# Optimization experiments

Measured on AMD Instinct MI355X. Metric: run time of the kernel, lower is better.

Reference implementation:

```python
import jax, jax.numpy as jnp
from jax import lax
import numpy as np

B, C, H, W = 32, 3, 224, 224
NUM_CLASSES = 100
K = 3  # kernel size
OUT1 = 32


def _bn(x, g, b, m, v, eps=1e-5):
    # eval-mode batchnorm over channel dim of NCHW
    inv = g / jnp.sqrt(v + eps)
    return x * inv[None, :, None, None] + (b - m * inv)[None, :, None, None]


def _conv(x, w, pad=1):
    return lax.conv_general_dilated(
        x, w, (1, 1), ((pad, pad), (pad, pad)),
        dimension_numbers=('NCHW', 'OIHW', 'NCHW'))


def _maxpool2(x):
    return lax.reduce_window(x, -jnp.inf, lax.max, (1, 1, 2, 2), (1, 1, 2, 2), 'VALID')


def setup_inputs() -> dict:
    key = jax.random.key(0)
    ks = jax.random.split(key, 32)
    n = lambda k, s, sc=0.05: jax.random.normal(k, s, jnp.float32) * sc
    u = lambda k, s: jax.random.uniform(k, s, jnp.float32, 0.5, 1.5)
    inp = {
        'x': jax.random.normal(ks[0], (B, C, H, W), jnp.float32),
        # weight_gen MLP: Linear(3,128)->ReLU->Linear(128,256)->ReLU->Linear(256, 32*3*3*3)
        'w1': n(ks[1], (128, C)), 'b1': n(ks[2], (128,)),
        'w2': n(ks[3], (256, 128)), 'b2': n(ks[4], (256,)),
        'w3': n(ks[5], (OUT1 * C * K * K, 256)), 'b3': n(ks[6], (OUT1 * C * K * K,)),
        # bias_gen: Linear(3, 32)
        'wb': n(ks[7], (OUT1, C)), 'bb': n(ks[8], (OUT1,)),
        'conv2_w': n(ks[9], (64, 32, 3, 3)), 'conv2_b': n(ks[10], (64,)),
        'conv3_w': n(ks[11], (128, 64, 3, 3)), 'conv3_b': n(ks[12], (128,)),
        'bn1_g': 1.0 + n(ks[13], (32,)), 'bn1_b': n(ks[14], (32,)), 'bn1_m': n(ks[15], (32,)), 'bn1_v': u(ks[16], (32,)),
        'bn2_g': 1.0 + n(ks[17], (64,)), 'bn2_b': n(ks[18], (64,)), 'bn2_m': n(ks[19], (64,)), 'bn2_v': u(ks[20], (64,)),
        'bn3_g': 1.0 + n(ks[21], (128,)), 'bn3_b': n(ks[22], (128,)), 'bn3_m': n(ks[23], (128,)), 'bn3_v': u(ks[24], (128,)),
        'fc_w': n(ks[25], (NUM_CLASSES, 128)), 'fc_b': n(ks[26], (NUM_CLASSES,)),
    }
    return inp


def reference(x, w1, b1, w2, b2, w3, b3, wb, bb, conv2_w, conv2_b, conv3_w, conv3_b,
              bn1_g, bn1_b, bn1_m, bn1_v, bn2_g, bn2_b, bn2_m, bn2_v,
              bn3_g, bn3_b, bn3_m, bn3_v, fc_w, fc_b):
    Bx = x.shape[0]
    # DynamicConv2D: channel indicator is all-ones since C == max_in_channels
    ind = jnp.ones((Bx, C), x.dtype)
    h = jax.nn.relu(ind @ w1.T + b1)
    h = jax.nn.relu(h @ w2.T + b2)
    dyn_w = (h @ w3.T + b3).reshape(Bx, OUT1, C, K, K)  # per-sample [O,I,k,k]
    dyn_b = ind @ wb.T + bb                             # per-sample [O]
    # vmap over batch: one single-image conv per sample with its own weights
    y = jax.vmap(lambda xi, wi, bi: _conv(xi[None], wi)[0] + bi[:, None, None])(x, dyn_w, dyn_b)
    y = jax.nn.relu(_bn(y, bn1_g, bn1_b, bn1_m, bn1_v))
    y = _maxpool2(y)
    y = jax.nn.relu(_bn(_conv(y, conv2_w) + conv2_b[None, :, None, None], bn2_g, bn2_b, bn2_m, bn2_v))
    y = _maxpool2(y)
    y = jax.nn.relu(_bn(_conv(y, conv3_w) + conv3_b[None, :, None, None], bn3_g, bn3_b, bn3_m, bn3_v))
    y = y.mean(axis=(2, 3))  # AdaptiveAvgPool2d((1,1)) + flatten
    # dropout is identity in eval
    return y @ fc_w.T + fc_b
```

## Files before the change

kernel.cpp:

```cpp
#include <hip/hip_runtime.h>
#include <hip/hip_bf16.h>

#define BATCH 32
#define HW1 224

typedef __attribute__((ext_vector_type(8))) short short8;
typedef __attribute__((ext_vector_type(4))) float floatx4;

static __device__ __forceinline__ unsigned short f2bf(float f) {
    unsigned int u = __float_as_uint(f);
    unsigned int r = (u + 0x7fffu + ((u >> 16) & 1u)) >> 16;
    return (unsigned short)r;
}

typedef __attribute__((address_space(1))) const unsigned int guint;
typedef __attribute__((address_space(3))) unsigned int suint;
static __device__ __forceinline__ void gload_lds16(const void* g, void* l) {
    __builtin_amdgcn_global_load_lds((guint*)g, (suint*)l, 16, 0, 0);
}

__global__ __launch_bounds__(256) void gen_dynw_repack(
    const float* __restrict__ w1, const float* __restrict__ b1,
    const float* __restrict__ w2, const float* __restrict__ b2,
    const float* __restrict__ w3, const float* __restrict__ b3,
    const float* __restrict__ conv2_w, const float* __restrict__ conv3_w,
    const float* __restrict__ wb, const float* __restrict__ bb,
    const float* __restrict__ conv2_b, const float* __restrict__ conv3_b,
    const float* __restrict__ bn1_g, const float* __restrict__ bn1_b,
    const float* __restrict__ bn1_m, const float* __restrict__ bn1_v,
    const float* __restrict__ bn2_g, const float* __restrict__ bn2_b,
    const float* __restrict__ bn2_m, const float* __restrict__ bn2_v,
    const float* __restrict__ bn3_g, const float* __restrict__ bn3_b,
    const float* __restrict__ bn3_m, const float* __restrict__ bn3_v,
    float* __restrict__ dwt,
    unsigned short* __restrict__ wrep2, unsigned short* __restrict__ wrep3,
    float* __restrict__ bn1_s, float* __restrict__ bn1_t,
    float* __restrict__ bn2_s, float* __restrict__ bn2_t,
    float* __restrict__ bn3_s, float* __restrict__ bn3_t,
    float* __restrict__ feat)
{
    __shared__ float h1s[128];
    __shared__ float h2s[256];
    const int blk = blockIdx.x;
    const int t = threadIdx.x;
    if (blk < 216) {
        if (t < 128) {
            float s = b1[t] + w1[t*3+0] + w1[t*3+1] + w1[t*3+2];
            h1s[t] = fmaxf(s, 0.f);
        }
        __syncthreads();
        {
            float s0 = b2[t], s1 = 0.f, s2 = 0.f, s3 = 0.f;
            const float* wr = w2 + (size_t)t*128;
#pragma unroll 4
            for (int k = 0; k < 128; k += 4) {
                float4 wv = *(const float4*)(wr + k);
                s0 = fmaf(wv.x, h1s[k  ], s0);
                s1 = fmaf(wv.y, h1s[k+1], s1);
                s2 = fmaf(wv.z, h1s[k+2], s2);
                s3 = fmaf(wv.w, h1s[k+3], s3);
            }
            h2s[t] = fmaxf((s0 + s1) + (s2 + s3), 0.f);
        }
        __syncthreads();
        const int wave = t >> 6, lane = t & 63;
        const int row = blk*4 + wave;
        float4 wv = *(const float4*)(w3 + (size_t)row*256 + lane*4);
        float4 hv = *(const float4*)&h2s[lane*4];
        float s = wv.x*hv.x + wv.y*hv.y + wv.z*hv.z + wv.w*hv.w;
#pragma unroll
        for (int m = 1; m < 64; m <<= 1) s += __shfl_xor(s, m);
        if (lane == 0) {
            int oc = row / 27, tap = row - oc*27;
            dwt[tap*32 + oc] = s + b3[row];
        }
    } else if (blk < 576) {
        const int i = (blk - 216)*256 + t;
        const int N2 = 9*64*32;
        if (i < N2) {
            int tp = i / (64*32); int rem = i - tp*(64*32);
            int oc = rem >> 5, ic = rem & 31;
            wrep2[i] = f2bf(conv2_w[(oc*32 + ic)*9 + tp]);
        } else {
            int j = i - N2;
            int tp = j / (128*64); int rem = j - tp*(128*64);
            int oc = rem >> 6, ic = rem & 63;
            wrep3[j] = f2bf(conv3_w[(oc*64 + ic)*9 + tp]);
        }
    } else {
        if (t < 32) {
            float dynb = bb[t] + wb[t*3+0] + wb[t*3+1] + wb[t*3+2];
            float s = bn1_g[t] / sqrtf(bn1_v[t] + 1e-5f);
            bn1_s[t] = s;
            bn1_t[t] = (dynb - bn1_m[t]) * s + bn1_b[t];
        }
        if (t < 64) {
            float s = bn2_g[t] / sqrtf(bn2_v[t] + 1e-5f);
            bn2_s[t] = s;
            bn2_t[t] = (conv2_b[t] - bn2_m[t]) * s + bn2_b[t];
        }
        if (t < 128) {
            float s = bn3_g[t] / sqrtf(bn3_v[t] + 1e-5f);
            bn3_s[t] = s;
            bn3_t[t] = (conv3_b[t] - bn3_m[t]) * s + bn3_b[t];
        }
        for (int i = t; i < BATCH*128; i += 256) feat[i] = 0.f;
    }
}

__global__ __launch_bounds__(256) void conv1_pool(
    const float* __restrict__ x, const float* __restrict__ dwt,
    const float* __restrict__ bn_s, const float* __restrict__ bn_t,
    unsigned short* __restrict__ act1)
{
    __shared__ __align__(16) unsigned short sp[18*18*4];
    __shared__ __align__(16) unsigned short swA[32*32];
    __shared__ __align__(16) unsigned short swB[32*32];

    const int tid = threadIdx.x;
    const int bx = blockIdx.x, by = blockIdx.y, b = blockIdx.z;
    const int gx0 = bx*16 - 1, gy0 = by*16 - 1;
    const float* xb = x + (size_t)b * 3 * HW1 * HW1;

    for (int i = tid; i < 1024; i += 256) { swA[i] = 0; swB[i] = 0; }

    float v[2][3];
#pragma unroll
    for (int k = 0; k < 2; ++k) {
        int i = tid + k*256;
        v[k][0] = 0.f; v[k][1] = 0.f; v[k][2] = 0.f;
        if (i < 324) {
            int r = i / 18, c = i - r*18;
            int gy = gy0 + r, gx = gx0 + c;
            if ((unsigned)gy < HW1 && (unsigned)gx < HW1) {
                const float* pp = xb + gy*HW1 + gx;
                v[k][0] = pp[0];
                v[k][1] = pp[HW1*HW1];
                v[k][2] = pp[2*HW1*HW1];
            }
        }
    }
#pragma unroll
    for (int k = 0; k < 2; ++k) {
        int i = tid + k*256;
        if (i < 324) {
            unsigned int lo = (unsigned int)f2bf(v[k][0]) |
                              ((unsigned int)f2bf(v[k][1]) << 16);
            unsigned int hi = (unsigned int)f2bf(v[k][2]);
            *(uint2*)&sp[i*4] = make_uint2(lo, hi);
        }
    }
    __syncthreads();

#pragma unroll
    for (int k = 0; k < 4; ++k) {
        int i = tid + k*256;
        if (i < 864) {
            int tap = i >> 5, oc = i & 31;
            int ic = tap / 9, kk = tap - ic*9;
            int ky = kk / 3, kx = kk - ky*3;
            unsigned short w = f2bf(dwt[i]);
            if (kk == 8)      swB[oc*32 + ic] = w;
            else if (kx < 2)  swA[oc*32 + ky*8 + kx*4 + ic] = w;
            else              swA[oc*32 + 3*8  + ky*4 + ic] = w;
        }
    }
    __syncthreads();

    const int lane = tid & 63, wave = tid >> 6;
    const int n = lane & 15, quad = lane >> 4;

    short8 afrA[2], afrB[2];
#pragma unroll
    for (int h = 0; h < 2; ++h) {
        afrA[h] = *(const short8*)&swA[((h*16 + n)*32) + quad*8];
        afrB[h] = *(const short8*)&swB[((h*16 + n)*32) + quad*8];
    }
    float4 sv[2], tv[2];
#pragma unroll
    for (int h = 0; h < 2; ++h) {
        sv[h] = *(const float4*)(bn_s + h*16 + quad*4);
        tv[h] = *(const float4*)(bn_t + h*16 + quad*4);
    }

    union U { short8 s8; uint2 u2[2]; };

    const int y0w = wave*4;
    float ev[2][4];

#pragma unroll
    for (int yi = 0; yi < 4; ++yi) {
        const int y = y0w + yi;
        int r0 = (quad < 3) ? (y + quad) : y;
        int c0 = (quad < 3) ? n : (n + 2);
        int r1 = (quad < 3) ? (y + quad) : (y + 1);
        int c1 = (quad < 3) ? (n + 1) : (n + 2);
        U bf1;
        bf1.u2[0] = *(const uint2*)&sp[(r0*18 + c0)*4];
        bf1.u2[1] = *(const uint2*)&sp[(r1*18 + c1)*4];
        U bf2;
        bf2.u2[0] = *(const uint2*)&sp[((y+2)*18 + (n+2))*4];
        bf2.u2[1] = bf2.u2[0];

        float vr[2][4];
#pragma unroll
        for (int h = 0; h < 2; ++h) {
            floatx4 acc = {0.f, 0.f, 0.f, 0.f};
            acc = __builtin_amdgcn_mfma_f32_16x16x32_bf16(afrA[h], bf1.s8, acc, 0, 0, 0);
            acc = __builtin_amdgcn_mfma_f32_16x16x32_bf16(afrB[h], bf2.s8, acc, 0, 0, 0);
            float sj[4] = {sv[h].x, sv[h].y, sv[h].z, sv[h].w};
            float tj[4] = {tv[h].x, tv[h].y, tv[h].z, tv[h].w};
#pragma unroll
            for (int j = 0; j < 4; ++j)
                vr[h][j] = fmaxf(fmaf(acc[j], sj[j], tj[j]), 0.f);
        }

        if ((yi & 1) == 0) {
#pragma unroll
            for (int h = 0; h < 2; ++h)
#pragma unroll
                for (int j = 0; j < 4; ++j) ev[h][j] = vr[h][j];
        } else {
            int py = by*8 + ((y0w + yi) >> 1);
            int px = bx*8 + (n >> 1);
            unsigned short* dstp =
                act1 + ((size_t)((b*112 + py)*112 + px))*32 + quad*4;
#pragma unroll
            for (int h = 0; h < 2; ++h) {
                unsigned int pk[2];
#pragma unroll
                for (int j = 0; j < 4; ++j) {
                    float m = fmaxf(vr[h][j], ev[h][j]);
                    m = fmaxf(m, __shfl_xor(m, 1));
                    unsigned short us = f2bf(m);
                    if (j & 1) pk[j >> 1] |= ((unsigned int)us) << 16;
                    else       pk[j >> 1]  = us;
                }
                if (!(n & 1)) *(uint2*)(dstp + h*16) = *(uint2*)pk;
            }
        }
    }
}

__global__ __launch_bounds__(256) void conv2_mfma(
    const unsigned short* __restrict__ act1,
    const unsigned short* __restrict__ wrep,
    const float* __restrict__ bn_s, const float* __restrict__ bn_t,
    unsigned short* __restrict__ act2)
{
    constexpr int IC = 32, OC = 64, H = 112;
    __shared__ __align__(16) short lds[4*18*18*8];

    const int tid = threadIdx.x;
    const int b = blockIdx.z;
    const int cx0 = blockIdx.x*16, cy0 = blockIdx.y*16;
    const unsigned short* ab = act1 + (size_t)b*H*H*IC;

    unsigned bad = 0;
    {
        int k = 0;
        for (int s = tid; s < 4*324; s += 256, ++k) {
            int ck = s / 324; int rem = s - ck*324;
            int y = rem / 18, xx = rem - y*18;
            int gy = cy0 - 1 + y, gx = cx0 - 1 + xx;
            if (!(((unsigned)gy < H) && ((unsigned)gx < H))) {
                bad |= 1u << k; gy = 0; gx = 0;
            }
            gload_lds16(ab + (size_t)(gy*H + gx)*IC + ck*8, &lds[s*8]);
        }
        if (bad) {
            asm volatile("s_waitcnt vmcnt(0)" ::: "memory");
            k = 0;
            for (int s = tid; s < 4*324; s += 256, ++k)
                if (bad & (1u << k)) {
                    uint4 z = {0u,0u,0u,0u};
                    *(uint4*)&lds[s*8] = z;
                }
        }
    }

    const int lane = tid & 63, wave = tid >> 6;
    const int n = lane & 15, quad = lane >> 4;
    const int oc0w = wave * 16;

    short8 afr[9];
#pragma unroll
    for (int t = 0; t < 9; ++t)
        afr[t] = *(const short8*)(wrep + (size_t)(t*OC + oc0w + n)*IC + quad*8);

    float4 sv = *(const float4*)(bn_s + oc0w + quad*4);
    float4 tv = *(const float4*)(bn_t + oc0w + quad*4);
    float sj[4] = {sv.x, sv.y, sv.z, sv.w};
    float tj[4] = {tv.x, tv.y, tv.z, tv.w};

    __syncthreads();

    floatx4 acc[3];
    float ev[4];

#pragma unroll
    for (int r = 0; r < 18; ++r) {
        const short* rp = &lds[((quad*18 + r)*18 + n)*8];
        short8 w0 = *(const short8*)(rp);
        short8 w1 = *(const short8*)(rp + 8);
        short8 w2 = *(const short8*)(rp + 16);

        if (r < 16) {
            floatx4 a = {0.f,0.f,0.f,0.f};
            a = __builtin_amdgcn_mfma_f32_16x16x32_bf16(afr[0], w0, a, 0, 0, 0);
            a = __builtin_amdgcn_mfma_f32_16x16x32_bf16(afr[1], w1, a, 0, 0, 0);
            a = __builtin_amdgcn_mfma_f32_16x16x32_bf16(afr[2], w2, a, 0, 0, 0);
            acc[r % 3] = a;
        }
        if (r >= 1 && r <= 16) {
            int y = r - 1;
            floatx4 a = acc[y % 3];
            a = __builtin_amdgcn_mfma_f32_16x16x32_bf16(afr[3], w0, a, 0, 0, 0);
            a = __builtin_amdgcn_mfma_f32_16x16x32_bf16(afr[4], w1, a, 0, 0, 0);
            a = __builtin_amdgcn_mfma_f32_16x16x32_bf16(afr[5], w2, a, 0, 0, 0);
            acc[y % 3] = a;
        }
        if (r >= 2) {
            int y = r - 2;
            floatx4 a = acc[y % 3];
            a = __builtin_amdgcn_mfma_f32_16x16x32_bf16(afr[6], w0, a, 0, 0, 0);
            a = __builtin_amdgcn_mfma_f32_16x16x32_bf16(afr[7], w1, a, 0, 0, 0);
            a = __builtin_amdgcn_mfma_f32_16x16x32_bf16(afr[8], w2, a, 0, 0, 0);

            float v[4];
#pragma unroll
            for (int j = 0; j < 4; ++j)
                v[j] = fmaxf(fmaf(a[j], sj[j], tj[j]), 0.f);

            if ((y & 1) == 0) {
#pragma unroll
                for (int j = 0; j < 4; ++j) ev[j] = v[j];
            } else {
                unsigned int pk[2];
#pragma unroll
                for (int j = 0; j < 4; ++j) {
                    float m = fmaxf(v[j], ev[j]);
                    m = fmaxf(m, __shfl_xor(m, 1));
                    unsigned short us = f2bf(m);
                    if (j & 1) pk[j >> 1] |= ((unsigned int)us) << 16;
                    else       pk[j >> 1]  = us;
                }
                if (!(n & 1)) {
                    int py = (cy0 >> 1) + (y >> 1), px = (cx0 >> 1) + (n >> 1);
                    unsigned short* dstp =
                        act2 + ((size_t)((b*56 + py)*56 + px))*OC + oc0w + quad*4;
                    *(uint2*)dstp = *(uint2*)pk;
                }
            }
        }
    }
}

__global__ __launch_bounds__(256) void conv3_mfma(
    const unsigned short* __restrict__ act2,
    const unsigned short* __restrict__ wrep,
    const float* __restrict__ bn_s, const float* __restrict__ bn_t,
    float* __restrict__ feat)
{
    constexpr int IC = 64, OC = 128, H = 56;
    __shared__ __align__(16) short lds[8*16*18*8];

    const int tid = threadIdx.x;
    const int b = blockIdx.z >> 1, half = blockIdx.z & 1;
    const int cx0 = blockIdx.x*16, cy0 = blockIdx.y*14;
    const unsigned short* ab = act2 + (size_t)b*H*H*IC;

    unsigned bad = 0;
    {
        int k = 0;
        for (int s = tid; s < 8*16*18; s += 256, ++k) {
            int ck = s / (16*18); int rem = s - ck*(16*18);
            int y = rem / 18, xx = rem - y*18;
            int gy = cy0 - 1 + y, gx = cx0 - 1 + xx;
            if (!(((unsigned)gy < H) && ((unsigned)gx < H))) {
                bad |= 1u << k; gy = 0; gx = 0;
            }
            gload_lds16(ab + (size_t)(gy*H + gx)*IC + ck*8, &lds[s*8]);
        }
        if (bad) {
            asm volatile("s_waitcnt vmcnt(0)" ::: "memory");
            k = 0;
            for (int s = tid; s < 8*16*18; s += 256, ++k)
                if (bad & (1u << k)) {
                    uint4 z = {0u,0u,0u,0u};
                    *(uint4*)&lds[s*8] = z;
                }
        }
    }

    const int lane = tid & 63, wave = tid >> 6;
    const int n = lane & 15, quad = lane >> 4;
    const int oc0w = half*64 + wave*16;

    short8 afr[18];
#pragma unroll
    for (int t = 0; t < 9; ++t)
#pragma unroll
        for (int kc = 0; kc < 2; ++kc)
            afr[t*2 + kc] = *(const short8*)(wrep + (size_t)(t*OC + oc0w + n)*IC + kc*32 + quad*8);

    float4 sv = *(const float4*)(bn_s + oc0w + quad*4);
    float4 tv = *(const float4*)(bn_t + oc0w + quad*4);
    float sj[4] = {sv.x, sv.y, sv.z, sv.w};
    float tj[4] = {tv.x, tv.y, tv.z, tv.w};

    __syncthreads();

    float sum[4] = {0.f, 0.f, 0.f, 0.f};
    const bool vx = (cx0 + n) < H;
    floatx4 acc[3];

#pragma unroll
    for (int r = 0; r < 16; ++r) {
        const short* p0 = &lds[((quad*16     + r)*18 + n)*8];
        const short* p1 = &lds[(((4+quad)*16 + r)*18 + n)*8];
        short8 a0 = *(const short8*)(p0);
        short8 a1 = *(const short8*)(p0 + 8);
        short8 a2 = *(const short8*)(p0 + 16);
        short8 b0 = *(const short8*)(p1);
        short8 b1 = *(const short8*)(p1 + 8);
        short8 b2 = *(const short8*)(p1 + 16);

        if (r < 14) {
            floatx4 a = {0.f,0.f,0.f,0.f};
            a = __builtin_amdgcn_mfma_f32_16x16x32_bf16(afr[0], a0, a, 0, 0, 0);
            a = __builtin_amdgcn_mfma_f32_16x16x32_bf16(afr[1], b0, a, 0, 0, 0);
            a = __builtin_amdgcn_mfma_f32_16x16x32_bf16(afr[2], a1, a, 0, 0, 0);
            a = __builtin_amdgcn_mfma_f32_16x16x32_bf16(afr[3], b1, a, 0, 0, 0);
            a = __builtin_amdgcn_mfma_f32_16x16x32_bf16(afr[4], a2, a, 0, 0, 0);
            a = __builtin_amdgcn_mfma_f32_16x16x32_bf16(afr[5], b2, a, 0, 0, 0);
            acc[r % 3] = a;
        }
        if (r >= 1 && r <= 14) {
            int y = r - 1;
            floatx4 a = acc[y % 3];
            a = __builtin_amdgcn_mfma_f32_16x16x32_bf16(afr[6],  a0, a, 0, 0, 0);
            a = __builtin_amdgcn_mfma_f32_16x16x32_bf16(afr[7],  b0, a, 0, 0, 0);
            a = __builtin_amdgcn_mfma_f32_16x16x32_bf16(afr[8],  a1, a, 0, 0, 0);
            a = __builtin_amdgcn_mfma_f32_16x16x32_bf16(afr[9],  b1, a, 0, 0, 0);
            a = __builtin_amdgcn_mfma_f32_16x16x32_bf16(afr[10], a2, a, 0, 0, 0);
            a = __builtin_amdgcn_mfma_f32_16x16x32_bf16(afr[11], b2, a, 0, 0, 0);
            acc[y % 3] = a;
        }
        if (r >= 2) {
            int y = r - 2;
            floatx4 a = acc[y % 3];
            a = __builtin_amdgcn_mfma_f32_16x16x32_bf16(afr[12], a0, a, 0, 0, 0);
            a = __builtin_amdgcn_mfma_f32_16x16x32_bf16(afr[13], b0, a, 0, 0, 0);
            a = __builtin_amdgcn_mfma_f32_16x16x32_bf16(afr[14], a1, a, 0, 0, 0);
            a = __builtin_amdgcn_mfma_f32_16x16x32_bf16(afr[15], b1, a, 0, 0, 0);
            a = __builtin_amdgcn_mfma_f32_16x16x32_bf16(afr[16], a2, a, 0, 0, 0);
            a = __builtin_amdgcn_mfma_f32_16x16x32_bf16(afr[17], b2, a, 0, 0, 0);
            if (vx) {
#pragma unroll
                for (int j = 0; j < 4; ++j)
                    sum[j] += fmaxf(fmaf(a[j], sj[j], tj[j]), 0.f);
            }
        }
    }
#pragma unroll
    for (int j = 0; j < 4; ++j) {
        sum[j] += __shfl_xor(sum[j], 1);
        sum[j] += __shfl_xor(sum[j], 2);
        sum[j] += __shfl_xor(sum[j], 4);
        sum[j] += __shfl_xor(sum[j], 8);
    }
    if (n == 0) {
#pragma unroll
        for (int j = 0; j < 4; ++j)
            atomicAdd(&feat[b*128 + oc0w + quad*4 + j], sum[j]);
    }
}

__global__ __launch_bounds__(256) void fc_kernel(
    const float* __restrict__ feat, const float* __restrict__ fc_w,
    const float* __restrict__ fc_b, float* __restrict__ out)
{
    int g = blockIdx.x * 16 + (threadIdx.x >> 4);
    int l = threadIdx.x & 15;
    if (g >= BATCH*100) return;
    int b = g / 100, n = g - b*100;
    const float* f = feat + b*128 + l*8;
    const float* w = fc_w + (size_t)n*128 + l*8;
    float4 f0 = *(const float4*)(f);
    float4 f1 = *(const float4*)(f + 4);
    float4 w0 = *(const float4*)(w);
    float4 w1 = *(const float4*)(w + 4);
    float s = f0.x*w0.x + f0.y*w0.y + f0.z*w0.z + f0.w*w0.w
            + f1.x*w1.x + f1.y*w1.y + f1.z*w1.z + f1.w*w1.w;
    s += __shfl_xor(s, 1);
    s += __shfl_xor(s, 2);
    s += __shfl_xor(s, 4);
    s += __shfl_xor(s, 8);
    if (l == 0) out[g] = s * (1.f/3136.f) + fc_b[n];
}

extern "C" void kernel_launch(void* const* d_in, const int* in_sizes, int n_in,
                              void* d_out, int out_size, void* d_ws, size_t ws_size,
                              hipStream_t stream)
{
    const float* x       = (const float*)d_in[0];
    const float* w1      = (const float*)d_in[1];
    const float* b1      = (const float*)d_in[2];
    const float* w2      = (const float*)d_in[3];
    const float* b2      = (const float*)d_in[4];
    const float* w3      = (const float*)d_in[5];
    const float* b3      = (const float*)d_in[6];
    const float* wb      = (const float*)d_in[7];
    const float* bb      = (const float*)d_in[8];
    const float* conv2_w = (const float*)d_in[9];
    const float* conv2_b = (const float*)d_in[10];
    const float* conv3_w = (const float*)d_in[11];
    const float* conv3_b = (const float*)d_in[12];
    const float* bn1_g = (const float*)d_in[13];
    const float* bn1_b = (const float*)d_in[14];
    const float* bn1_m = (const float*)d_in[15];
    const float* bn1_v = (const float*)d_in[16];
    const float* bn2_g = (const float*)d_in[17];
    const float* bn2_b = (const float*)d_in[18];
    const float* bn2_m = (const float*)d_in[19];
    const float* bn2_v = (const float*)d_in[20];
    const float* bn3_g = (const float*)d_in[21];
    const float* bn3_b = (const float*)d_in[22];
    const float* bn3_m = (const float*)d_in[23];
    const float* bn3_v = (const float*)d_in[24];
    const float* fc_w  = (const float*)d_in[25];
    const float* fc_b  = (const float*)d_in[26];
    float* out = (float*)d_out;

    char* wsb = (char*)d_ws;
    float* ws    = (float*)d_ws;
    float* dwt   = ws;
    float* bn1_s = ws + 864;
    float* bn1_t = ws + 896;
    float* bn2_s = ws + 928;
    float* bn2_t = ws + 992;
    float* bn3_s = ws + 1056;
    float* bn3_t = ws + 1184;
    float* feat  = ws + 1312;
    unsigned short* wrep2 = (unsigned short*)(wsb + 32768);
    unsigned short* wrep3 = (unsigned short*)(wsb + 69632);
    unsigned short* act1  = (unsigned short*)(wsb + 262144);
    unsigned short* act2  = (unsigned short*)(wsb + 262144 + 25690112);

    gen_dynw_repack<<<577, 256, 0, stream>>>(
        w1, b1, w2, b2, w3, b3, conv2_w, conv3_w,
        wb, bb, conv2_b, conv3_b,
        bn1_g, bn1_b, bn1_m, bn1_v, bn2_g, bn2_b, bn2_m, bn2_v,
        bn3_g, bn3_b, bn3_m, bn3_v,
        dwt, wrep2, wrep3,
        bn1_s, bn1_t, bn2_s, bn2_t, bn3_s, bn3_t, feat);

    conv1_pool<<<dim3(14, 14, BATCH), 256, 0, stream>>>(
        x, dwt, bn1_s, bn1_t, act1);

    conv2_mfma<<<dim3(7, 7, BATCH), 256, 0, stream>>>(
        act1, wrep2, bn2_s, bn2_t, act2);

    conv3_mfma<<<dim3(4, 4, BATCH*2), 256, 0, stream>>>(
        act2, wrep3, bn3_s, bn3_t, feat);

    fc_kernel<<<200, 256, 0, stream>>>(feat, fc_w, fc_b, out);
}
```

Baseline: 182.2 us.

## Split conv2/conv3 waves by row group and two output-channel subtiles for B-fragment reuse

In conv2 and conv3, each wave previously covered all rows of the tile for a single 16-channel output slice. Now waves are arranged as 2 row groups by 2 channel groups, and each wave computes two 16-channel subtiles. Every LDS B-fragment read therefore feeds two MFMAs, which roughly halves LDS read traffic per MFMA. The cost is that each row group recomputes 2 halo rows and the wave holds twice as many weight fragments in registers, which may raise VGPR pressure (36 short8 in conv3).

After: 194.0 us. 1.07x slower.

```diff
diff --git a/kernel.cpp b/kernel.cpp
--- a/kernel.cpp
+++ b/kernel.cpp
@@ -18,6 +18,8 @@
 static __device__ __forceinline__ void gload_lds16(const void* g, void* l) {
     __builtin_amdgcn_global_load_lds((guint*)g, (suint*)l, 16, 0, 0);
 }
+
+#define MFMA(A, B, C) __builtin_amdgcn_mfma_f32_16x16x32_bf16((A), (B), (C), 0, 0, 0)
 
 __global__ __launch_bounds__(256) void gen_dynw_repack(
     const float* __restrict__ w1, const float* __restrict__ b1,
@@ -206,8 +208,8 @@
 #pragma unroll
         for (int h = 0; h < 2; ++h) {
             floatx4 acc = {0.f, 0.f, 0.f, 0.f};
-            acc = __builtin_amdgcn_mfma_f32_16x16x32_bf16(afrA[h], bf1.s8, acc, 0, 0, 0);
-            acc = __builtin_amdgcn_mfma_f32_16x16x32_bf16(afrB[h], bf2.s8, acc, 0, 0, 0);
+            acc = MFMA(afrA[h], bf1.s8, acc);
+            acc = MFMA(afrB[h], bf2.s8, acc);
             float sj[4] = {sv[h].x, sv[h].y, sv[h].z, sv[h].w};
             float tj[4] = {tv[h].x, tv[h].y, tv[h].z, tv[h].w};
 #pragma unroll
@@ -281,75 +283,96 @@
 
     const int lane = tid & 63, wave = tid >> 6;
     const int n = lane & 15, quad = lane >> 4;
-    const int oc0w = wave * 16;
-
-    short8 afr[9];
+    const int rgrp = wave >> 1;
+    const int ocg  = wave & 1;
+
+    short8 afr[9][2];
 #pragma unroll
     for (int t = 0; t < 9; ++t)
-        afr[t] = *(const short8*)(wrep + (size_t)(t*OC + oc0w + n)*IC + quad*8);
-
-    float4 sv = *(const float4*)(bn_s + oc0w + quad*4);
-    float4 tv = *(const float4*)(bn_t + oc0w + quad*4);
-    float sj[4] = {sv.x, sv.y, sv.z, sv.w};
-    float tj[4] = {tv.x, tv.y, tv.z, tv.w};
+#pragma unroll
+        for (int sub = 0; sub < 2; ++sub)
+            afr[t][sub] = *(const short8*)(wrep +
+                (size_t)(t*OC + ocg*32 + sub*16 + n)*IC + quad*8);
+
+    float sj[2][4], tj[2][4];
+#pragma unroll
+    for (int sub = 0; sub < 2; ++sub) {
+        float4 sv = *(const float4*)(bn_s + ocg*32 + sub*16 + quad*4);
+        float4 tv = *(const float4*)(bn_t + ocg*32 + sub*16 + quad*4);
+        sj[sub][0] = sv.x; sj[sub][1] = sv.y; sj[sub][2] = sv.z; sj[sub][3] = sv.w;
+        tj[sub][0] = tv.x; tj[sub][1] = tv.y; tj[sub][2] = tv.z; tj[sub][3] = tv.w;
+    }
 
     __syncthreads();
 
-    floatx4 acc[3];
-    float ev[4];
-
-#pragma unroll
-    for (int r = 0; r < 18; ++r) {
-        const short* rp = &lds[((quad*18 + r)*18 + n)*8];
+    floatx4 acc[3][2];
+    float ev[2][4];
+
+#pragma unroll
+    for (int r = 0; r < 10; ++r) {
+        const int rr = rgrp*8 + r;
+        const short* rp = &lds[((quad*18 + rr)*18 + n)*8];
         short8 w0 = *(const short8*)(rp);
         short8 w1 = *(const short8*)(rp + 8);
         short8 w2 = *(const short8*)(rp + 16);
 
-        if (r < 16) {
-            floatx4 a = {0.f,0.f,0.f,0.f};
-            a = __builtin_amdgcn_mfma_f32_16x16x32_bf16(afr[0], w0, a, 0, 0, 0);
-            a = __builtin_amdgcn_mfma_f32_16x16x32_bf16(afr[1], w1, a, 0, 0, 0);
-            a = __builtin_amdgcn_mfma_f32_16x16x32_bf16(afr[2], w2, a, 0, 0, 0);
-            acc[r % 3] = a;
-        }
-        if (r >= 1 && r <= 16) {
+        if (r < 8) {
+#pragma unroll
+            for (int sub = 0; sub < 2; ++sub) {
+                floatx4 a = {0.f,0.f,0.f,0.f};
+                a = MFMA(afr[0][sub], w0, a);
+                a = MFMA(afr[1][sub], w1, a);
+                a = MFMA(afr[2][sub], w2, a);
+                acc[r % 3][sub] = a;
+            }
+        }
+        if (r >= 1 && r <= 8) {
             int y = r - 1;
-            floatx4 a = acc[y % 3];
-            a = __builtin_amdgcn_mfma_f32_16x16x32_bf16(afr[3], w0, a, 0, 0, 0);
-            a = __builtin_amdgcn_mfma_f32_16x16x32_bf16(afr[4], w1, a, 0, 0, 0);
-            a = __builtin_amdgcn_mfma_f32_16x16x32_bf16(afr[5], w2, a, 0, 0, 0);
-            acc[y % 3] = a;
+#pragma unroll
+            for (int sub = 0; sub < 2; ++sub) {
+                floatx4 a = acc[y % 3][sub];
+                a = MFMA(afr[3][sub], w0, a);
+                a = MFMA(afr[4][sub], w1, a);
+                a = MFMA(afr[5][sub], w2, a);
+                acc[y % 3][sub] = a;
+            }
         }
         if (r >= 2) {
             int y = r - 2;
-            floatx4 a = acc[y % 3];
-            a = __builtin_amdgcn_mfma_f32_16x16x32_bf16(afr[6], w0, a, 0, 0, 0);
-            a = __builtin_amdgcn_mfma_f32_16x16x32_bf16(afr[7], w1, a, 0, 0, 0);
-            a = __builtin_amdgcn_mfma_f32_16x16x32_bf16(afr[8], w2, a, 0, 0, 0);
-
-            float v[4];
-#pragma unroll
-            for (int j = 0; j < 4; ++j)
-                v[j] = fmaxf(fmaf(a[j], sj[j], tj[j]), 0.f);
+            float v[2][4];
+#pragma unroll
+            for (int sub = 0; sub < 2; ++sub) {
+                floatx4 a = acc[y % 3][sub];
+                a = MFMA(afr[6][sub], w0, a);
+                a = MFMA(afr[7][sub], w1, a);
+                a = MFMA(afr[8][sub], w2, a);
+#pragma unroll
+                for (int j = 0; j < 4; ++j)
+                    v[sub][j] = fmaxf(fmaf(a[j], sj[sub][j], tj[sub][j]), 0.f);
+            }
 
             if ((y & 1) == 0) {
 #pragma unroll
-                for (int j = 0; j < 4; ++j) ev[j] = v[j];
+                for (int sub = 0; sub < 2; ++sub)
+#pragma unroll
+                    for (int j = 0; j < 4; ++j) ev[sub][j] = v[sub][j];
             } else {
-                unsigned int pk[2];
-#pragma unroll
-                for (int j = 0; j < 4; ++j) {
-                    float m = fmaxf(v[j], ev[j]);
-                    m = fmaxf(m, __shfl_xor(m, 1));
-                    unsigned short us = f2bf(m);
-                    if (j & 1) pk[j >> 1] |= ((unsigned int)us) << 16;
-                    else       pk[j >> 1]  = us;
-                }
-                if (!(n & 1)) {
-                    int py = (cy0 >> 1) + (y >> 1), px = (cx0 >> 1) + (n >> 1);
-                    unsigned short* dstp =
-                        act2 + ((size_t)((b*56 + py)*56 + px))*OC + oc0w + quad*4;
-                    *(uint2*)dstp = *(uint2*)pk;
+                int yg = rgrp*8 + y;
+                int py = (cy0 >> 1) + (yg >> 1), px = (cx0 >> 1) + (n >> 1);
+                unsigned short* dstp =
+                    act2 + ((size_t)((b*56 + py)*56 + px))*OC + ocg*32 + quad*4;
+#pragma unroll
+                for (int sub = 0; sub < 2; ++sub) {
+                    unsigned int pk[2];
+#pragma unroll
+                    for (int j = 0; j < 4; ++j) {
+                        float m = fmaxf(v[sub][j], ev[sub][j]);
+                        m = fmaxf(m, __shfl_xor(m, 1));
+                        unsigned short us = f2bf(m);
+                        if (j & 1) pk[j >> 1] |= ((unsigned int)us) << 16;
+                        else       pk[j >> 1]  = us;
+                    }
+                    if (!(n & 1)) *(uint2*)(dstp + sub*16) = *(uint2*)pk;
                 }
             }
         }
@@ -395,30 +418,40 @@
 
     const int lane = tid & 63, wave = tid >> 6;
     const int n = lane & 15, quad = lane >> 4;
-    const int oc0w = half*64 + wave*16;
-
-    short8 afr[18];
+    const int rgrp = wave >> 1;
+    const int ocs  = wave & 1;
+    const int oc0  = half*64 + ocs*32;
+
+    short8 afr[9][2][2];
 #pragma unroll
     for (int t = 0; t < 9; ++t)
 #pragma unroll
         for (int kc = 0; kc < 2; ++kc)
-            afr[t*2 + kc] = *(const short8*)(wrep + (size_t)(t*OC + oc0w + n)*IC + kc*32 + quad*8);
-
-    float4 sv = *(const float4*)(bn_s + oc0w + quad*4);
-    float4 tv = *(const float4*)(bn_t + oc0w + quad*4);
-    float sj[4] = {sv.x, sv.y, sv.z, sv.w};
-    float tj[4] = {tv.x, tv.y, tv.z, tv.w};
+#pragma unroll
+            for (int sub = 0; sub < 2; ++sub)
+                afr[t][kc][sub] = *(const short8*)(wrep +
+                    (size_t)(t*OC + oc0 + sub*16 + n)*IC + kc*32 + quad*8);
+
+    float sj[2][4], tj[2][4];
+#pragma unroll
+    for (int sub = 0; sub < 2; ++sub) {
+        float4 sv = *(const float4*)(bn_s + oc0 + sub*16 + quad*4);
+        float4 tv = *(const float4*)(bn_t + oc0 + sub*16 + quad*4);
+        sj[sub][0] = sv.x; sj[sub][1] = sv.y; sj[sub][2] = sv.z; sj[sub][3] = sv.w;
+        tj[sub][0] = tv.x; tj[sub][1] = tv.y; tj[sub][2] = tv.z; tj[sub][3] = tv.w;
+    }
 
     __syncthreads();
 
-    float sum[4] = {0.f, 0.f, 0.f, 0.f};
+    float sum[2][4] = {{0.f,0.f,0.f,0.f},{0.f,0.f,0.f,0.f}};
     const bool vx = (cx0 + n) < H;
-    floatx4 acc[3];
-
-#pragma unroll
-    for (int r = 0; r < 16; ++r) {
-        const short* p0 = &lds[((quad*16     + r)*18 + n)*8];
-        const short* p1 = &lds[(((4+quad)*16 + r)*18 + n)*8];
+    floatx4 acc[3][2];
+
+#pragma unroll
+    for (int r = 0; r < 9; ++r) {
+        const int rr = rgrp*7 + r;
+        const short* p0 = &lds[((quad*16     + rr)*18 + n)*8];
+        const short* p1 = &lds[(((4+quad)*16 + rr)*18 + n)*8];
         short8 a0 = *(const short8*)(p0);
         short8 a1 = *(const short8*)(p0 + 8);
         short8 a2 = *(const short8*)(p0 + 16);
@@ -426,54 +459,67 @@
         short8 b1 = *(const short8*)(p1 + 8);
         short8 b2 = *(const short8*)(p1 + 16);
 
-        if (r < 14) {
-            floatx4 a = {0.f,0.f,0.f,0.f};
-            a = __builtin_amdgcn_mfma_f32_16x16x32_bf16(afr[0], a0, a, 0, 0, 0);
-            a = __builtin_amdgcn_mfma_f32_16x16x32_bf16(afr[1], b0, a, 0, 0, 0);
-            a = __builtin_amdgcn_mfma_f32_16x16x32_bf16(afr[2], a1, a, 0, 0, 0);
-            a = __builtin_amdgcn_mfma_f32_16x16x32_bf16(afr[3], b1, a, 0, 0, 0);
-            a = __builtin_amdgcn_mfma_f32_16x16x32_bf16(afr[4], a2, a, 0, 0, 0);
-            a = __builtin_amdgcn_mfma_f32_16x16x32_bf16(afr[5], b2, a, 0, 0, 0);
-            acc[r % 3] = a;
-        }
-        if (r >= 1 && r <= 14) {
+        if (r < 7) {
+#pragma unroll
+            for (int sub = 0; sub < 2; ++sub) {
+                floatx4 a = {0.f,0.f,0.f,0.f};
+                a = MFMA(afr[0][0][sub], a0, a);
+                a = MFMA(afr[0][1][sub], b0, a);
+                a = MFMA(afr[1][0][sub], a1, a);
+                a = MFMA(afr[1][1][sub], b1, a);
+                a = MFMA(afr[2][0][sub], a2, a);
+                a = MFMA(afr[2][1][sub], b2, a);
+                acc[r % 3][sub] = a;
+            }
+        }
+        if (r >= 1 && r <= 7) {
             int y = r - 1;
-            floatx4 a = acc[y % 3];
-            a = __builtin_amdgcn_mfma_f32_16x16x32_bf16(afr[6],  a0, a, 0, 0, 0);
-            a = __builtin_amdgcn_mfma_f32_16x16x32_bf16(afr[7],  b0, a, 0, 0, 0);
-            a = __builtin_amdgcn_mfma_f32_16x16x32_bf16(afr[8],  a1, a, 0, 0, 0);
-            a = __builtin_amdgcn_mfma_f32_16x16x32_bf16(afr[9],  b1, a, 0, 0, 0);
-            a = __builtin_amdgcn_mfma_f32_16x16x32_bf16(afr[10], a2, a, 0, 0, 0);
-            a = __builtin_amdgcn_mfma_f32_16x16x32_bf16(afr[11], b2, a, 0, 0, 0);
-            acc[y % 3] = a;
+#pragma unroll
+            for (int sub = 0; sub < 2; ++sub) {
+                floatx4 a = acc[y % 3][sub];
+                a = MFMA(afr[3][0][sub], a0, a);
+                a = MFMA(afr[3][1][sub], b0, a);
+                a = MFMA(afr[4][0][sub], a1, a);
+                a = MFMA(afr[4][1][sub], b1, a);
+                a = MFMA(afr[5][0][sub], a2, a);
+                a = MFMA(afr[5][1][sub], b2, a);
+                acc[y % 3][sub] = a;
+            }
         }
         if (r >= 2) {
             int y = r - 2;
-            floatx4 a = acc[y % 3];
-            a = __builtin_amdgcn_mfma_f32_16x16x32_bf16(afr[12], a0, a, 0, 0, 0);
-            a = __builtin_amdgcn_mfma_f32_16x16x32_bf16(afr[13], b0, a, 0, 0, 0);
-            a = __builtin_amdgcn_mfma_f32_16x16x32_bf16(afr[14], a1, a, 0, 0, 0);
-            a = __builtin_amdgcn_mfma_f32_16x16x32_bf16(afr[15], b1, a, 0, 0, 0);
-            a = __builtin_amdgcn_mfma_f32_16x16x32_bf16(afr[16], a2, a, 0, 0, 0);
-            a = __builtin_amdgcn_mfma_f32_16x16x32_bf16(afr[17], b2, a, 0, 0, 0);
-            if (vx) {
-#pragma unroll
-                for (int j = 0; j < 4; ++j)
-                    sum[j] += fmaxf(fmaf(a[j], sj[j], tj[j]), 0.f);
-            }
-        }
-    }
-#pragma unroll
-    for (int j = 0; j < 4; ++j) {
-        sum[j] += __shfl_xor(sum[j], 1);
-        sum[j] += __shfl_xor(sum[j], 2);
-        sum[j] += __shfl_xor(sum[j], 4);
-        sum[j] += __shfl_xor(sum[j], 8);
-    }
+#pragma unroll
+            for (int sub = 0; sub < 2; ++sub) {
+                floatx4 a = acc[y % 3][sub];
+                a = MFMA(afr[6][0][sub], a0, a);
+                a = MFMA(afr[6][1][sub], b0, a);
+                a = MFMA(afr[7][0][sub], a1, a);
+                a = MFMA(afr[7][1][sub], b1, a);
+                a = MFMA(afr[8][0][sub], a2, a);
+                a = MFMA(afr[8][1][sub], b2, a);
+                if (vx) {
+#pragma unroll
+                    for (int j = 0; j < 4; ++j)
+                        sum[sub][j] += fmaxf(fmaf(a[j], sj[sub][j], tj[sub][j]), 0.f);
+                }
+            }
+        }
+    }
+#pragma unroll
+    for (int sub = 0; sub < 2; ++sub)
+#pragma unroll
+        for (int j = 0; j < 4; ++j) {
+            sum[sub][j] += __shfl_xor(sum[sub][j], 1);
+            sum[sub][j] += __shfl_xor(sum[sub][j], 2);
+            sum[sub][j] += __shfl_xor(sum[sub][j], 4);
+            sum[sub][j] += __shfl_xor(sum[sub][j], 8);
+        }
     if (n == 0) {
 #pragma unroll
-        for (int j = 0; j < 4; ++j)
-            atomicAdd(&feat[b*128 + oc0w + quad*4 + j], sum[j]);
+        for (int sub = 0; sub < 2; ++sub)
+#pragma unroll
+            for (int j = 0; j < 4; ++j)
+                atomicAdd(&feat[b*128 + oc0 + sub*16 + quad*4 + j], sum[sub][j]);
     }
 }
 
```
